# Kernel tuning notes

Measured on AMD Instinct MI355X. Metric: run time of the kernel, lower is better.

The kernel has to match this reference:

```python
import jax, jax.numpy as jnp
import numpy as np

EPS = 1e-5
KERNELS = [3, 3, 5, 7]  # 2*i+1 for i>=1, first layer k=3


def _conv_relu_bn(x, w, b, gamma, beta, rmean, rvar):
    # x: [B, Cin, S], w: [Cout, Cin, K]
    k = w.shape[-1]
    y = jax.lax.conv_general_dilated(
        x, w, window_strides=(1,), padding=[(k // 2, k // 2)],
        dimension_numbers=("NCW", "OIW", "NCW"))
    y = y + b[None, :, None]
    y = jax.nn.relu(y)
    # BatchNorm1d in inference mode (running stats)
    inv = gamma[None, :, None] / jnp.sqrt(rvar[None, :, None] + EPS)
    return (y - rmean[None, :, None]) * inv + beta[None, :, None]


def setup_inputs() -> dict:
    key = jax.random.key(0)
    ks = jax.random.split(key, 32)
    B, S = 128, 8192
    inp = {"x": jax.random.normal(ks[0], (B, 4, S), dtype=jnp.float32)}
    cin = 4
    for i, k in enumerate(KERNELS):
        inp[f"w{i}"] = jax.random.normal(ks[1 + i], (32, cin, k), dtype=jnp.float32) * 0.1
        inp[f"b{i}"] = jnp.zeros((32,), jnp.float32)
        inp[f"g{i}"] = jnp.ones((32,), jnp.float32)   # BN gamma
        inp[f"bb{i}"] = jnp.zeros((32,), jnp.float32)  # BN beta
        inp[f"rm{i}"] = jnp.zeros((32,), jnp.float32)  # running mean
        inp[f"rv{i}"] = jnp.ones((32,), jnp.float32)   # running var
        cin = 32
    inp["fw1"] = jax.random.normal(ks[10], (16, 32), dtype=jnp.float32) * 0.1
    inp["fb1"] = jnp.zeros((16,), jnp.float32)
    inp["fw2"] = jax.random.normal(ks[11], (1, 16), dtype=jnp.float32) * 0.1
    inp["fb2"] = jnp.zeros((1,), jnp.float32)
    return inp


def reference(x,
              w0, b0, g0, bb0, rm0, rv0,
              w1, b1, g1, bb1, rm1, rv1,
              w2, b2, g2, bb2, rm2, rv2,
              w3, b3, g3, bb3, rm3, rv3,
              fw1, fb1, fw2, fb2):
    x = _conv_relu_bn(x, w0, b0, g0, bb0, rm0, rv0)
    x = _conv_relu_bn(x, w1, b1, g1, bb1, rm1, rv1)
    x = _conv_relu_bn(x, w2, b2, g2, bb2, rm2, rv2)
    x = _conv_relu_bn(x, w3, b3, g3, bb3, rm3, rv3)
    # [B, 32, S] -> [B, S, 32]; the original per-timestep MLP loop is one batched GEMM
    h = jnp.einsum("bcs,hc->bsh", x, fw1) + fb1
    h = jax.nn.relu(h)  # Dropout(0.1) is identity in eval
    out = jnp.einsum("bsh,oh->bso", h, fw2) + fb2
    return out[..., 0]  # squeeze(-1) -> [B, S]
```

## Files before the change

### kernel.cpp

```cpp
#include <hip/hip_runtime.h>

#define SEQ    8192
#define S_TILE 180
#define NROW   198
#define CS     1608
#define NTHR   256
#define NREC   37
#define BN_HALFOFF (NREC*512)

typedef __attribute__((ext_vector_type(8))) _Float16 half8;
typedef __attribute__((ext_vector_type(4))) _Float16 half4v;
typedef __attribute__((ext_vector_type(4))) float    f32x4;

__device__ __forceinline__ int uni(int v){ return __builtin_amdgcn_readfirstlane(v); }

template<int K>
__device__ __forceinline__ float fold_bias(const float* __restrict__ W, int co,
    const float* __restrict__ gp, const float* __restrict__ bbp,
    const float* __restrict__ rmp, const float* __restrict__ rvp)
{
    float acc = 0.f;
#pragma unroll
    for (int ci = 0; ci < 32; ++ci) {
        float sp = gp[ci] * rsqrtf(rvp[ci] + 1e-5f);
        float tp = bbp[ci] - rmp[ci]*sp;
        float wsum = 0.f;
#pragma unroll
        for (int tap = 0; tap < K; ++tap) wsum += W[(co*32 + ci)*K + tap];
        acc += wsum * tp;
    }
    return acc;
}

extern "C" __global__ void prep_kernel(
    const float* w0, const float* w1, const float* w2, const float* w3,
    const float* b0, const float* g0, const float* bb0, const float* rm0, const float* rv0,
    const float* b1, const float* g1, const float* bb1, const float* rm1, const float* rv1,
    const float* b2, const float* g2, const float* bb2, const float* rm2, const float* rv2,
    const float* b3, const float* g3, const float* bb3, const float* rm3, const float* rv3,
    const float* fw1, const float* fb1, _Float16* ws)
{
    const int tid = threadIdx.x;
    const int rec = blockIdx.x;
    if (rec < NREC) {
        if (tid < 64) {
            const int lane = tid;
            const float* W; const float *gp = nullptr, *rvp = nullptr; int CIN, K, r2;
            if      (rec < 6)  { W = w0;  CIN = 4;  K = 3; r2 = rec;      }
            else if (rec < 12) { W = w1;  CIN = 32; K = 3; r2 = rec - 6;  gp = g0; rvp = rv0; }
            else if (rec < 22) { W = w2;  CIN = 32; K = 5; r2 = rec - 12; gp = g1; rvp = rv1; }
            else if (rec < 36) { W = w3;  CIN = 32; K = 7; r2 = rec - 22; gp = g2; rvp = rv2; }
            else               { W = fw1; CIN = 32; K = 1; r2 = 0;        gp = g3; rvp = rv3; }
            int tap = r2 >> 1, mh = r2 & 1;
            int co  = mh*16 + (lane & 15);
            int ci0 = (lane >> 4) * 8;
            half8 h;
#pragma unroll
            for (int j = 0; j < 8; ++j) {
                int ci = ci0 + j;
                float wv = (ci < CIN) ? W[(co*CIN + ci)*K + tap] : 0.0f;
                if (gp) wv *= gp[ci & 31] * rsqrtf(rvp[ci & 31] + 1e-5f);
                h[j] = (_Float16)wv;
            }
            *(half8*)(ws + rec*512 + lane*8) = h;
        }
    } else {
        float* fa = (float*)(ws + BN_HALFOFF);
        if (tid < 128) {
            int l = tid >> 5, co = tid & 31;
            const float *g, *bb, *rm, *rv, *bi;
            if      (l == 0) { g=g0; bb=bb0; rm=rm0; rv=rv0; bi=b0; }
            else if (l == 1) { g=g1; bb=bb1; rm=rm1; rv=rv1; bi=b1; }
            else if (l == 2) { g=g2; bb=bb2; rm=rm2; rv=rv2; bi=b2; }
            else             { g=g3; bb=bb3; rm=rm3; rv=rv3; bi=b3; }
            float s = g[co] * rsqrtf(rv[co] + 1e-5f);
            float t = bb[co] - rm[co]*s;
            float bias = bi[co];
            if      (l == 1) bias += fold_bias<3>(w1, co, g0, bb0, rm0, rv0);
            else if (l == 2) bias += fold_bias<5>(w2, co, g1, bb1, rm1, rv1);
            else if (l == 3) bias += fold_bias<7>(w3, co, g2, bb2, rm2, rv2);
            fa[(l*32 + co)*2 + 0] = bias;
            fa[(l*32 + co)*2 + 1] = -t / s;
        } else if (tid < 144) {
            int hh = tid - 128;
            float acc = fb1[hh];
#pragma unroll
            for (int c = 0; c < 32; ++c) {
                float s3 = g3[c] * rsqrtf(rv3[c] + 1e-5f);
                float t3 = bb3[c] - rm3[c]*s3;
                acc += fw1[hh*32 + c] * t3;
            }
            fa[256 + hh] = acc;
        }
    }
}

template<int K, int DOFF, bool BC0>
__device__ __forceinline__ void conv_layer(
    const _Float16* __restrict__ rec, const float2* __restrict__ bo,
    const _Float16* in, _Float16* outb, int s0, int ntb, int lane)
{
    const int q = lane >> 4, n = lane & 15;
    const _Float16* bbase = in + (BC0 ? 0 : q*CS) + (ntb*16 + n)*8;

    f32x4 acc[3][2];
#pragma unroll
    for (int nt = 0; nt < 3; ++nt)
#pragma unroll
        for (int mh = 0; mh < 2; ++mh) acc[nt][mh] = (f32x4){0.f, 0.f, 0.f, 0.f};

#pragma unroll
    for (int tap = 0; tap < K; ++tap) {
        half8 a0 = *(const half8*)(rec + (tap*2 + 0)*512 + lane*8);
        half8 a1 = *(const half8*)(rec + (tap*2 + 1)*512 + lane*8);
#pragma unroll
        for (int nt = 0; nt < 3; ++nt) {
            half8 bf = *(const half8*)(bbase + nt*128 + tap*8);
            acc[nt][0] = __builtin_amdgcn_mfma_f32_16x16x32_f16(a0, bf, acc[nt][0], 0, 0, 0);
            acc[nt][1] = __builtin_amdgcn_mfma_f32_16x16x32_f16(a1, bf, acc[nt][1], 0, 0, 0);
        }
    }

#pragma unroll
    for (int nt = 0; nt < 3; ++nt) {
        int pos = (ntb + nt)*16 + n;
        bool oob = (unsigned)(s0 + DOFF + pos) >= SEQ;
#pragma unroll
        for (int mh = 0; mh < 2; ++mh) {
            int co0 = mh*16 + q*4;
            half4v hv;
#pragma unroll
            for (int r = 0; r < 4; ++r) {
                float2 p = bo[co0 + r];
                float v = fmaxf(acc[nt][mh][r] + p.x, 0.0f);
                if (oob) v = p.y;
                hv[r] = (_Float16)v;
            }
            int cb = mh*2 + (q >> 1);
            *(half4v*)(outb + cb*CS + pos*8 + (q & 1)*4) = hv;
        }
    }
}

extern "C" __global__ void __launch_bounds__(NTHR, 6)
dnashape_mfma(const float* __restrict__ x, const _Float16* __restrict__ ws,
              const float* __restrict__ fw2, const float* __restrict__ fb2,
              float* __restrict__ out)
{
    __shared__ _Float16 bufA[4*CS];
    __shared__ _Float16 bufB[4*CS];

    const int tid  = threadIdx.x;
    const int tile = blockIdx.x;
    const int s0   = tile * S_TILE;
    const int b    = blockIdx.y;

    {
        const float* xb = x + b*4*SEQ;
        for (int li = tid; li < NROW; li += NTHR) {
            int sg = s0 - 7 + li;
            bool ok = (unsigned)sg < SEQ;
            float v0 = ok ? xb[0*SEQ + sg] : 0.f;
            float v1 = ok ? xb[1*SEQ + sg] : 0.f;
            float v2 = ok ? xb[2*SEQ + sg] : 0.f;
            float v3 = ok ? xb[3*SEQ + sg] : 0.f;
            half8 h0 = {(_Float16)v0, (_Float16)v1, (_Float16)v2, (_Float16)v3, 0, 0, 0, 0};
            *(half8*)(&bufB[0*CS + li*8]) = h0;
        }
        if (tid < 32) {
            const half8 z8 = {0,0,0,0,0,0,0,0};
            *(half8*)(&bufA[(tid >> 3)*CS + (192 + (tid & 7))*8]) = z8;
        }
    }
    __syncthreads();

    const int lane = tid & 63;
    const int wv   = uni(tid >> 6);
    const int ntb  = wv * 3;
    const float*  fa = (const float*)(ws + BN_HALFOFF);
    const float2* bo = (const float2*)fa;

    conv_layer<3, -6, true >(ws +  0*512, bo +  0, bufB, bufA, s0, ntb, lane);
    __syncthreads();
    conv_layer<3, -5, false>(ws +  6*512, bo + 32, bufA, bufB, s0, ntb, lane);
    __syncthreads();
    conv_layer<5, -3, false>(ws + 12*512, bo + 64, bufB, bufA, s0, ntb, lane);
    __syncthreads();
    conv_layer<7,  0, false>(ws + 22*512, bo + 96, bufA, bufB, s0, ntb, lane);
    __syncthreads();

    {
        const int q = lane >> 4, n = lane & 15;
        half8 am = *(const half8*)(ws + 36*512 + lane*8);
        float fb1v[4], fw2v[4];
#pragma unroll
        for (int r = 0; r < 4; ++r) { fb1v[r] = fa[256 + q*4 + r]; fw2v[r] = fw2[q*4 + r]; }
        float fb2v = fb2[0];
#pragma unroll
        for (int nt = 0; nt < 3; ++nt) {
            int pos = (ntb + nt)*16 + n;
            half8 bf = *(const half8*)(&bufB[q*CS + pos*8]);
            f32x4 d = {0.f, 0.f, 0.f, 0.f};
            d = __builtin_amdgcn_mfma_f32_16x16x32_f16(am, bf, d, 0, 0, 0);
            float part = 0.f;
#pragma unroll
            for (int r = 0; r < 4; ++r) part += fmaxf(d[r] + fb1v[r], 0.f)*fw2v[r];
            part += __shfl_xor(part, 16, 64);
            part += __shfl_xor(part, 32, 64);
            if (lane < 16) {
                int g = s0 + pos;
                if (pos < S_TILE && g < SEQ) out[b*SEQ + g] = part + fb2v;
            }
        }
    }
}

extern "C" void kernel_launch(void* const* d_in, const int* in_sizes, int n_in,
                              void* d_out, int out_size, void* d_ws, size_t ws_size,
                              hipStream_t stream) {
    const float* p[29];
    for (int i = 0; i < 29; ++i) p[i] = (const float*)d_in[i];
    _Float16* ws = (_Float16*)d_ws;

    prep_kernel<<<dim3(NREC + 1), 144, 0, stream>>>(
        p[1], p[7], p[13], p[19],
        p[2], p[3], p[4], p[5], p[6],
        p[8], p[9], p[10], p[11], p[12],
        p[14], p[15], p[16], p[17], p[18],
        p[20], p[21], p[22], p[23], p[24],
        p[25], p[26], ws);

    dim3 grid((SEQ + S_TILE - 1) / S_TILE, 128);
    dnashape_mfma<<<grid, NTHR, 0, stream>>>(p[0], (const _Float16*)ws,
                                             p[27], p[28], (float*)d_out);
}
```

Measured before the change: 167.6 us.

## Pack first-layer taps into MFMA K dimension and software-pipeline tap loads

The first conv layer (Cin=4, K=3) now packs all 12 tap×channel inputs into the MFMA reduction dimension, so it runs one MFMA pair per tile instead of three. The staging of input x into LDS writes the tap-shifted im2col rows, and the weight prep packs w0 to match. The other conv layers also prefetch the next tap's A/B fragments before issuing the current MFMAs, to hide LDS latency. The cost is more global loads during x staging and extra register pressure from the double-buffered fragments.

```diff
diff --git a/kernel.cpp b/kernel.cpp
--- a/kernel.cpp
+++ b/kernel.cpp
@@ -5,7 +5,7 @@
 #define NROW   198
 #define CS     1608
 #define NTHR   256
-#define NREC   37
+#define NREC   33
 #define BN_HALFOFF (NREC*512)
 
 typedef __attribute__((ext_vector_type(8))) _Float16 half8;
@@ -45,22 +45,31 @@
     if (rec < NREC) {
         if (tid < 64) {
             const int lane = tid;
-            const float* W; const float *gp = nullptr, *rvp = nullptr; int CIN, K, r2;
-            if      (rec < 6)  { W = w0;  CIN = 4;  K = 3; r2 = rec;      }
-            else if (rec < 12) { W = w1;  CIN = 32; K = 3; r2 = rec - 6;  gp = g0; rvp = rv0; }
-            else if (rec < 22) { W = w2;  CIN = 32; K = 5; r2 = rec - 12; gp = g1; rvp = rv1; }
-            else if (rec < 36) { W = w3;  CIN = 32; K = 7; r2 = rec - 22; gp = g2; rvp = rv2; }
-            else               { W = fw1; CIN = 32; K = 1; r2 = 0;        gp = g3; rvp = rv3; }
-            int tap = r2 >> 1, mh = r2 & 1;
-            int co  = mh*16 + (lane & 15);
-            int ci0 = (lane >> 4) * 8;
             half8 h;
-#pragma unroll
-            for (int j = 0; j < 8; ++j) {
-                int ci = ci0 + j;
-                float wv = (ci < CIN) ? W[(co*CIN + ci)*K + tap] : 0.0f;
-                if (gp) wv *= gp[ci & 31] * rsqrtf(rvp[ci & 31] + 1e-5f);
-                h[j] = (_Float16)wv;
+            if (rec < 2) {
+                int co = rec*16 + (lane & 15);
+#pragma unroll
+                for (int j = 0; j < 8; ++j) {
+                    int k = (lane >> 4)*8 + j;
+                    float wv = (k < 12) ? w0[(co*4 + (k & 3))*3 + (k >> 2)] : 0.0f;
+                    h[j] = (_Float16)wv;
+                }
+            } else {
+                const float* W; const float *gp, *rvp; int K, r2;
+                if      (rec < 8)  { W = w1;  K = 3; r2 = rec - 2;  gp = g0; rvp = rv0; }
+                else if (rec < 18) { W = w2;  K = 5; r2 = rec - 8;  gp = g1; rvp = rv1; }
+                else if (rec < 32) { W = w3;  K = 7; r2 = rec - 18; gp = g2; rvp = rv2; }
+                else               { W = fw1; K = 1; r2 = 0;        gp = g3; rvp = rv3; }
+                int tap = r2 >> 1, mh = r2 & 1;
+                int co  = mh*16 + (lane & 15);
+                int ci0 = (lane >> 4) * 8;
+#pragma unroll
+                for (int j = 0; j < 8; ++j) {
+                    int ci = ci0 + j;
+                    float wv = W[(co*32 + ci)*K + tap];
+                    wv *= gp[ci] * rsqrtf(rvp[ci] + 1e-5f);
+                    h[j] = (_Float16)wv;
+                }
             }
             *(half8*)(ws + rec*512 + lane*8) = h;
         }
@@ -95,36 +104,14 @@
     }
 }
 
-template<int K, int DOFF, bool BC0>
-__device__ __forceinline__ void conv_layer(
-    const _Float16* __restrict__ rec, const float2* __restrict__ bo,
-    const _Float16* in, _Float16* outb, int s0, int ntb, int lane)
-{
-    const int q = lane >> 4, n = lane & 15;
-    const _Float16* bbase = in + (BC0 ? 0 : q*CS) + (ntb*16 + n)*8;
-
-    f32x4 acc[3][2];
-#pragma unroll
-    for (int nt = 0; nt < 3; ++nt)
-#pragma unroll
-        for (int mh = 0; mh < 2; ++mh) acc[nt][mh] = (f32x4){0.f, 0.f, 0.f, 0.f};
-
-#pragma unroll
-    for (int tap = 0; tap < K; ++tap) {
-        half8 a0 = *(const half8*)(rec + (tap*2 + 0)*512 + lane*8);
-        half8 a1 = *(const half8*)(rec + (tap*2 + 1)*512 + lane*8);
-#pragma unroll
-        for (int nt = 0; nt < 3; ++nt) {
-            half8 bf = *(const half8*)(bbase + nt*128 + tap*8);
-            acc[nt][0] = __builtin_amdgcn_mfma_f32_16x16x32_f16(a0, bf, acc[nt][0], 0, 0, 0);
-            acc[nt][1] = __builtin_amdgcn_mfma_f32_16x16x32_f16(a1, bf, acc[nt][1], 0, 0, 0);
-        }
-    }
-
+__device__ __forceinline__ void conv_epi(
+    const f32x4 (*acc)[2], const float2* __restrict__ bo,
+    _Float16* outb, int s0, int doff, int ntb, int q, int n)
+{
 #pragma unroll
     for (int nt = 0; nt < 3; ++nt) {
         int pos = (ntb + nt)*16 + n;
-        bool oob = (unsigned)(s0 + DOFF + pos) >= SEQ;
+        bool oob = (unsigned)(s0 + doff + pos) >= SEQ;
 #pragma unroll
         for (int mh = 0; mh < 2; ++mh) {
             int co0 = mh*16 + q*4;
@@ -142,6 +129,72 @@
     }
 }
 
+template<int K, int DOFF>
+__device__ __forceinline__ void conv_layer(
+    const _Float16* __restrict__ rec, const float2* __restrict__ bo,
+    const _Float16* in, _Float16* outb, int s0, int ntb, int lane)
+{
+    const int q = lane >> 4, n = lane & 15;
+    const _Float16* bbase = in + q*CS + (ntb*16 + n)*8;
+
+    f32x4 acc[3][2];
+#pragma unroll
+    for (int nt = 0; nt < 3; ++nt)
+#pragma unroll
+        for (int mh = 0; mh < 2; ++mh) acc[nt][mh] = (f32x4){0.f, 0.f, 0.f, 0.f};
+
+    half8 a0 = *(const half8*)(rec + 0*512 + lane*8);
+    half8 a1 = *(const half8*)(rec + 1*512 + lane*8);
+    half8 b0 = *(const half8*)(bbase + 0*128);
+    half8 b1 = *(const half8*)(bbase + 1*128);
+    half8 b2 = *(const half8*)(bbase + 2*128);
+
+#pragma unroll
+    for (int tap = 0; tap < K; ++tap) {
+        half8 na0, na1, nb0, nb1, nb2;
+        if (tap + 1 < K) {
+            na0 = *(const half8*)(rec + ((tap+1)*2 + 0)*512 + lane*8);
+            na1 = *(const half8*)(rec + ((tap+1)*2 + 1)*512 + lane*8);
+            nb0 = *(const half8*)(bbase + 0*128 + (tap+1)*8);
+            nb1 = *(const half8*)(bbase + 1*128 + (tap+1)*8);
+            nb2 = *(const half8*)(bbase + 2*128 + (tap+1)*8);
+        }
+        acc[0][0] = __builtin_amdgcn_mfma_f32_16x16x32_f16(a0, b0, acc[0][0], 0, 0, 0);
+        acc[0][1] = __builtin_amdgcn_mfma_f32_16x16x32_f16(a1, b0, acc[0][1], 0, 0, 0);
+        acc[1][0] = __builtin_amdgcn_mfma_f32_16x16x32_f16(a0, b1, acc[1][0], 0, 0, 0);
+        acc[1][1] = __builtin_amdgcn_mfma_f32_16x16x32_f16(a1, b1, acc[1][1], 0, 0, 0);
+        acc[2][0] = __builtin_amdgcn_mfma_f32_16x16x32_f16(a0, b2, acc[2][0], 0, 0, 0);
+        acc[2][1] = __builtin_amdgcn_mfma_f32_16x16x32_f16(a1, b2, acc[2][1], 0, 0, 0);
+        if (tap + 1 < K) { a0 = na0; a1 = na1; b0 = nb0; b1 = nb1; b2 = nb2; }
+    }
+    conv_epi(acc, bo, outb, s0, DOFF, ntb, q, n);
+}
+
+__device__ __forceinline__ void conv_layer0(
+    const _Float16* __restrict__ rec, const float2* __restrict__ bo,
+    const _Float16* in, _Float16* outb, int s0, int ntb, int lane)
+{
+    const int q = lane >> 4, n = lane & 15;
+    const _Float16* bbase = in + (q & 1)*CS + (ntb*16 + n)*8;
+
+    half8 a0 = *(const half8*)(rec + 0*512 + lane*8);
+    half8 a1 = *(const half8*)(rec + 1*512 + lane*8);
+
+    f32x4 acc[3][2];
+#pragma unroll
+    for (int nt = 0; nt < 3; ++nt)
+#pragma unroll
+        for (int mh = 0; mh < 2; ++mh) acc[nt][mh] = (f32x4){0.f, 0.f, 0.f, 0.f};
+
+#pragma unroll
+    for (int nt = 0; nt < 3; ++nt) {
+        half8 bf = *(const half8*)(bbase + nt*128);
+        acc[nt][0] = __builtin_amdgcn_mfma_f32_16x16x32_f16(a0, bf, acc[nt][0], 0, 0, 0);
+        acc[nt][1] = __builtin_amdgcn_mfma_f32_16x16x32_f16(a1, bf, acc[nt][1], 0, 0, 0);
+    }
+    conv_epi(acc, bo, outb, s0, -6, ntb, q, n);
+}
+
 extern "C" __global__ void __launch_bounds__(NTHR, 6)
 dnashape_mfma(const float* __restrict__ x, const _Float16* __restrict__ ws,
               const float* __restrict__ fw2, const float* __restrict__ fb2,
@@ -158,14 +211,19 @@
     {
         const float* xb = x + b*4*SEQ;
         for (int li = tid; li < NROW; li += NTHR) {
-            int sg = s0 - 7 + li;
-            bool ok = (unsigned)sg < SEQ;
-            float v0 = ok ? xb[0*SEQ + sg] : 0.f;
-            float v1 = ok ? xb[1*SEQ + sg] : 0.f;
-            float v2 = ok ? xb[2*SEQ + sg] : 0.f;
-            float v3 = ok ? xb[3*SEQ + sg] : 0.f;
-            half8 h0 = {(_Float16)v0, (_Float16)v1, (_Float16)v2, (_Float16)v3, 0, 0, 0, 0};
-            *(half8*)(&bufB[0*CS + li*8]) = h0;
+            _Float16 h[16];
+#pragma unroll
+            for (int tap = 0; tap < 3; ++tap) {
+                int sg = s0 - 7 + li + tap;
+                bool ok = (unsigned)sg < SEQ;
+#pragma unroll
+                for (int ci = 0; ci < 4; ++ci)
+                    h[tap*4 + ci] = (_Float16)(ok ? xb[ci*SEQ + sg] : 0.f);
+            }
+#pragma unroll
+            for (int j = 12; j < 16; ++j) h[j] = (_Float16)0.f;
+            *(half8*)(&bufB[0*CS + li*8]) = *(half8*)(h);
+            *(half8*)(&bufB[1*CS + li*8]) = *(half8*)(h + 8);
         }
         if (tid < 32) {
             const half8 z8 = {0,0,0,0,0,0,0,0};
@@ -180,18 +238,18 @@
     const float*  fa = (const float*)(ws + BN_HALFOFF);
     const float2* bo = (const float2*)fa;
 
-    conv_layer<3, -6, true >(ws +  0*512, bo +  0, bufB, bufA, s0, ntb, lane);
-    __syncthreads();
-    conv_layer<3, -5, false>(ws +  6*512, bo + 32, bufA, bufB, s0, ntb, lane);
-    __syncthreads();
-    conv_layer<5, -3, false>(ws + 12*512, bo + 64, bufB, bufA, s0, ntb, lane);
-    __syncthreads();
-    conv_layer<7,  0, false>(ws + 22*512, bo + 96, bufA, bufB, s0, ntb, lane);
+    conv_layer0             (ws,           bo,      bufB, bufA, s0, ntb, lane);
+    __syncthreads();
+    conv_layer<3, -5>(ws +  2*512,   bo + 32, bufA, bufB, s0, ntb, lane);
+    __syncthreads();
+    conv_layer<5, -3>(ws +  8*512,   bo + 64, bufB, bufA, s0, ntb, lane);
+    __syncthreads();
+    conv_layer<7,  0>(ws + 18*512,   bo + 96, bufA, bufB, s0, ntb, lane);
     __syncthreads();
 
     {
         const int q = lane >> 4, n = lane & 15;
-        half8 am = *(const half8*)(ws + 36*512 + lane*8);
+        half8 am = *(const half8*)(ws + 32*512 + lane*8);
         float fb1v[4], fw2v[4];
 #pragma unroll
         for (int r = 0; r < 4; ++r) { fb1v[r] = fa[256 + q*4 + r]; fw2v[r] = fw2[q*4 + r]; }
```

Result: slower. 173.3 us (+3.4%).
